# Performance work log

Hardware: AMD Instinct MI355X
Metric: run time of the kernel (lower is better)

## Reference

```python
import jax, jax.numpy as jnp
import numpy as np

B, D, H, E, NDIFF = 4096, 2048, 4096, 8, 3
TOPK = 2


def setup_inputs() -> dict:
    key = jax.random.key(0)
    ks = jax.random.split(key, 8)
    x = jax.random.normal(ks[0], (B, D), dtype=jnp.float32)
    difficulty_labels = jax.random.randint(ks[1], (B,), 0, NDIFF)
    emb = jax.random.normal(ks[2], (NDIFF, D), dtype=jnp.float32) * 0.02
    gate_W = jax.random.normal(ks[3], (E, 2 * D), dtype=jnp.float32) / np.sqrt(2.0 * D)
    gate_b = jnp.zeros((E,), dtype=jnp.float32)
    expert_W = jax.random.normal(ks[4], (E, H, D), dtype=jnp.float32) / np.sqrt(D)
    expert_b = jax.random.normal(ks[5], (E, H), dtype=jnp.float32) * 0.01
    return {"x": x, "difficulty_labels": difficulty_labels, "emb": emb,
            "gate_W": gate_W, "gate_b": gate_b,
            "expert_W": expert_W, "expert_b": expert_b}


def reference(x, difficulty_labels, emb, gate_W, gate_b, expert_W, expert_b):
    # gating: concat token features with difficulty embedding
    gate_in = jnp.concatenate([x, emb[difficulty_labels]], axis=1)       # [B, 2D]
    gate_logits = gate_in @ gate_W.T + gate_b                             # [B, E]
    topw, topk_idx = jax.lax.top_k(gate_logits, TOPK)                     # [B, 2]
    topk_probs = jax.nn.softmax(topw, axis=1)                             # [B, 2]
    # per-token combine weight for each expert (top-2 indices are distinct)
    combine = jnp.zeros((x.shape[0], E), dtype=x.dtype)
    combine = combine.at[jnp.arange(x.shape[0])[:, None], topk_idx].add(topk_probs)
    # dispatch/compute/combine: tokens with combine weight 0 contribute 0,
    # matching the masked gather/scatter-add of the original.
    out = jnp.zeros((x.shape[0], expert_W.shape[1]), dtype=x.dtype)
    for e in range(E):  # small fixed loop over experts
        y = x @ expert_W[e].T + expert_b[e]                               # [B, H]
        out = out + y * combine[:, e:e + 1]
    return (out, topk_idx)
```

## Files before the change

kernel.cpp:

```cpp
#include <hip/hip_runtime.h>
#include <hip/hip_bf16.h>

#define B_TOK 4096
#define DIM   2048
#define HID   4096
#define NEXP  8
#define CAP   4224

#define BM 128
#define BN 128
#define BK 64

typedef short  bf16x8 __attribute__((ext_vector_type(8)));
typedef unsigned short us16x8 __attribute__((ext_vector_type(8)));
typedef float  f32x4  __attribute__((ext_vector_type(4)));

__device__ __forceinline__ unsigned short f2bf(float f) {
    unsigned u = __builtin_bit_cast(unsigned, f);
    u += 0x7fffu + ((u >> 16) & 1u);
    return (unsigned short)(u >> 16);
}

__device__ __forceinline__ void async_copy16(const void* g, void* l) {
    __builtin_amdgcn_global_load_lds(
        (const __attribute__((address_space(1))) unsigned*)g,
        (__attribute__((address_space(3))) unsigned*)l, 16, 0, 0);
}

__global__ __launch_bounds__(256) void cvt_kernel(
    const float* __restrict__ src, unsigned short* __restrict__ dst, long n) {
    long i = ((long)blockIdx.x * 256 + threadIdx.x) * 8;
    if (i >= n) return;
    float4 v0 = *(const float4*)(src + i);
    float4 v1 = *(const float4*)(src + i + 4);
    us16x8 o = { f2bf(v0.x), f2bf(v0.y), f2bf(v0.z), f2bf(v0.w),
                 f2bf(v1.x), f2bf(v1.y), f2bf(v1.z), f2bf(v1.w) };
    *(us16x8*)(dst + i) = o;
}

__global__ __launch_bounds__(256) void compute_c_kernel(
    const float* __restrict__ emb, const float* __restrict__ gate_W,
    const float* __restrict__ gate_b, float* __restrict__ cbuf) {
    int wave = (blockIdx.x * blockDim.x + threadIdx.x) >> 6;
    int lane = threadIdx.x & 63;
    if (wave >= 24) return;
    int n = wave >> 3, e = wave & 7;
    const float4* er = (const float4*)(emb + (size_t)n * DIM);
    const float4* wr = (const float4*)(gate_W + (size_t)e * 2 * DIM + DIM);
    float acc = 0.f;
    for (int c = lane; c < DIM / 4; c += 64) {
        float4 a = er[c], b = wr[c];
        acc += a.x * b.x + a.y * b.y + a.z * b.z + a.w * b.w;
    }
    #pragma unroll
    for (int off = 32; off; off >>= 1) acc += __shfl_down(acc, off, 64);
    if (lane == 0) cbuf[n * 8 + e] = acc + gate_b[e];
}

__global__ __launch_bounds__(256) void gating_kernel(
    const float* __restrict__ x, const int* __restrict__ labels,
    const float* __restrict__ gate_W, const float* __restrict__ cbuf,
    int* __restrict__ counts, int* __restrict__ tlist,
    float* __restrict__ wlist, float* __restrict__ out_idx) {
    int wave = threadIdx.x >> 6, lane = threadIdx.x & 63;
    int b = blockIdx.x * 4 + wave;
    const float4* xr  = (const float4*)(x + (size_t)b * DIM);
    const float4* gw4 = (const float4*)gate_W;
    float acc[8] = {0.f, 0.f, 0.f, 0.f, 0.f, 0.f, 0.f, 0.f};
    for (int c = lane; c < DIM / 4; c += 64) {
        float4 xv = xr[c];
        #pragma unroll
        for (int e = 0; e < 8; ++e) {
            float4 wv = gw4[e * (2 * DIM / 4) + c];
            acc[e] += xv.x * wv.x + xv.y * wv.y + xv.z * wv.z + xv.w * wv.w;
        }
    }
    #pragma unroll
    for (int off = 32; off; off >>= 1) {
        #pragma unroll
        for (int e = 0; e < 8; ++e) acc[e] += __shfl_down(acc[e], off, 64);
    }
    if (lane == 0) {
        int lbl = labels[b];
        float lg[8];
        #pragma unroll
        for (int e = 0; e < 8; ++e) lg[e] = acc[e] + cbuf[lbl * 8 + e];
        int e0 = 0; float t0 = lg[0];
        #pragma unroll
        for (int e = 1; e < 8; ++e) if (lg[e] > t0) { t0 = lg[e]; e0 = e; }
        int e1 = -1; float t1 = -1e30f;
        #pragma unroll
        for (int e = 0; e < 8; ++e)
            if (e != e0 && lg[e] > t1) { t1 = lg[e]; e1 = e; }
        float w0 = 1.f / (1.f + __expf(t1 - t0));
        float w1 = 1.f - w0;
        int p0 = atomicAdd(&counts[e0], 1);
        int p1 = atomicAdd(&counts[e1], 1);
        tlist[e0 * CAP + p0] = b; wlist[e0 * CAP + p0] = w0;
        tlist[e1 * CAP + p1] = b; wlist[e1 * CAP + p1] = w1;
        out_idx[2 * b]     = (float)e0;
        out_idx[2 * b + 1] = (float)e1;
    }
}

__global__ void pad_kernel(const int* __restrict__ counts,
                           int* __restrict__ tlist, float* __restrict__ wlist) {
    int e = blockIdx.x, c = counts[e];
    int padded = (c + BM - 1) & ~(BM - 1);
    int i = c + threadIdx.x;
    if (i < padded) { tlist[e * CAP + i] = 0; wlist[e * CAP + i] = 0.f; }
}

__global__ __launch_bounds__(256) void moe_gemm_kernel(
    const unsigned short* __restrict__ xb, const unsigned short* __restrict__ Wb,
    const float* __restrict__ expert_b, const int* __restrict__ counts,
    const int* __restrict__ tlist, const float* __restrict__ wlist,
    float* __restrict__ out) {
    const int e  = blockIdx.z;
    const int m0 = blockIdx.y * BM;
    if (m0 >= counts[e]) return;
    const int n0 = blockIdx.x * BN;

    __shared__ unsigned short As[BM * BK];
    __shared__ unsigned short Bs[BN * BK];
    __shared__ int   toks[BM];
    __shared__ float wts[BM];

    const int t = threadIdx.x;
    if (t < BM) {
        toks[t] = tlist[e * CAP + m0 + t];
        wts[t]  = wlist[e * CAP + m0 + t];
    }
    __syncthreads();

    const int lane = t & 63, wave = t >> 6;
    const int rowc = lane >> 3;
    const int gsw  = ((lane & 7) ^ rowc) * 8;

    const unsigned short* gA[4];
    const unsigned short* gB[4];
    unsigned short* ldsA[4];
    unsigned short* ldsB[4];
    #pragma unroll
    for (int j = 0; j < 4; ++j) {
        int row = wave * 32 + j * 8 + rowc;
        gA[j] = xb + (size_t)toks[row] * DIM + gsw;
        gB[j] = Wb + ((size_t)e * HID + n0 + row) * DIM + gsw;
        ldsA[j] = As + (wave * 32 + j * 8) * BK;
        ldsB[j] = Bs + (wave * 32 + j * 8) * BK;
    }

    const int wm = wave >> 1, wn = wave & 1;
    const int r = lane & 15, quad = lane >> 4;

    f32x4 acc[4][4] = {};

    for (int k0 = 0; k0 < DIM; k0 += BK) {
        #pragma unroll
        for (int j = 0; j < 4; ++j) async_copy16(gA[j] + k0, ldsA[j]);
        #pragma unroll
        for (int j = 0; j < 4; ++j) async_copy16(gB[j] + k0, ldsB[j]);
        __syncthreads();
        #pragma unroll
        for (int kk = 0; kk < 2; ++kk) {
            bf16x8 af[4], bfr[4];
            const int pg = ((kk * 4 + quad) ^ (r & 7)) * 8;
            #pragma unroll
            for (int i = 0; i < 4; ++i) {
                af[i]  = *(const bf16x8*)&As[(wm * 64 + i * 16 + r) * BK + pg];
                bfr[i] = *(const bf16x8*)&Bs[(wn * 64 + i * 16 + r) * BK + pg];
            }
            #pragma unroll
            for (int im = 0; im < 4; ++im)
                #pragma unroll
                for (int in = 0; in < 4; ++in)
                    acc[im][in] = __builtin_amdgcn_mfma_f32_16x16x32_bf16(
                        af[im], bfr[in], acc[im][in], 0, 0, 0);
        }
        __syncthreads();
    }

    const float* eb = expert_b + (size_t)e * HID;
    #pragma unroll
    for (int in = 0; in < 4; ++in) {
        int col = n0 + wn * 64 + in * 16 + r;
        float bias = eb[col];
        #pragma unroll
        for (int im = 0; im < 4; ++im) {
            int rowb = wm * 64 + im * 16 + quad * 4;
            #pragma unroll
            for (int r4 = 0; r4 < 4; ++r4) {
                int row = rowb + r4;
                float w = wts[row];
                if (w != 0.f)
                    atomicAdd(out + (size_t)toks[row] * HID + col,
                              w * (acc[im][in][r4] + bias));
            }
        }
    }
}

extern "C" void kernel_launch(void* const* d_in, const int* in_sizes, int n_in,
                              void* d_out, int out_size, void* d_ws, size_t ws_size,
                              hipStream_t stream) {
    const float* x        = (const float*)d_in[0];
    const int*   labels   = (const int*)  d_in[1];
    const float* emb      = (const float*)d_in[2];
    const float* gate_W   = (const float*)d_in[3];
    const float* gate_b   = (const float*)d_in[4];
    const float* expert_W = (const float*)d_in[5];
    const float* expert_b = (const float*)d_in[6];
    float* out = (float*)d_out;

    char* ws = (char*)d_ws;
    int*   counts = (int*)ws;
    float* cbuf   = (float*)(ws + 128);
    int*   tlist  = (int*)(ws + 512);
    float* wlist  = (float*)(ws + 512 + NEXP * CAP * 4);
    unsigned short* xb = (unsigned short*)(ws + 512 + 2 * NEXP * CAP * 4);
    unsigned short* Wb = xb + (size_t)B_TOK * DIM;

    hipMemsetAsync(counts, 0, 8 * sizeof(int), stream);
    hipMemsetAsync(out, 0, (size_t)B_TOK * HID * sizeof(float), stream);

    cvt_kernel<<<(B_TOK * DIM) / (8 * 256), 256, 0, stream>>>(
        x, xb, (long)B_TOK * DIM);
    cvt_kernel<<<(NEXP * HID * DIM) / (8 * 256), 256, 0, stream>>>(
        expert_W, Wb, (long)NEXP * HID * DIM);
    compute_c_kernel<<<6, 256, 0, stream>>>(emb, gate_W, gate_b, cbuf);
    gating_kernel<<<B_TOK / 4, 256, 0, stream>>>(
        x, labels, gate_W, cbuf, counts, tlist, wlist,
        out + (size_t)B_TOK * HID);
    pad_kernel<<<NEXP, BM, 0, stream>>>(counts, tlist, wlist);
    moe_gemm_kernel<<<dim3(HID / BN, B_TOK / BM, NEXP), 256, 0, stream>>>(
        xb, Wb, expert_b, counts, tlist, wlist, out);
}
```

Measured before the change: 891.5 us.

## Replace atomic scatter-add with rank-slot stores plus combine kernel; double-buffer GEMM

The GEMM no longer atomically adds weighted results into a zeroed output. Each token's first-ranked expert result goes straight into out and its second into a y1 workspace, with padded rows sent to a trash buffer. A new combine kernel then applies bias and gating weights. The GEMM main loop also moves to BK=32 with double-buffered LDS staging and a launch-bounds occupancy hint. This removes the output memset and the fp32 atomics, at the cost of an extra 64MB buffer and a full read/write combine pass. The trash row is shared by all padded rows and written concurrently, which is a benign race.

```diff
diff --git a/kernel.cpp b/kernel.cpp
--- a/kernel.cpp
+++ b/kernel.cpp
@@ -9,7 +9,8 @@
 
 #define BM 128
 #define BN 128
-#define BK 64
+#define BK 32
+#define KITER (DIM / BK)
 
 typedef short  bf16x8 __attribute__((ext_vector_type(8)));
 typedef unsigned short us16x8 __attribute__((ext_vector_type(8)));
@@ -60,8 +61,10 @@
 __global__ __launch_bounds__(256) void gating_kernel(
     const float* __restrict__ x, const int* __restrict__ labels,
     const float* __restrict__ gate_W, const float* __restrict__ cbuf,
-    int* __restrict__ counts, int* __restrict__ tlist,
-    float* __restrict__ wlist, float* __restrict__ out_idx) {
+    int* __restrict__ counts, int* __restrict__ tlist, int* __restrict__ rlist,
+    float* __restrict__ wA, float* __restrict__ wB,
+    int* __restrict__ eA, int* __restrict__ eB,
+    float* __restrict__ out_idx) {
     int wave = threadIdx.x >> 6, lane = threadIdx.x & 63;
     int b = blockIdx.x * 4 + wave;
     const float4* xr  = (const float4*)(x + (size_t)b * DIM);
@@ -96,107 +99,141 @@
         float w1 = 1.f - w0;
         int p0 = atomicAdd(&counts[e0], 1);
         int p1 = atomicAdd(&counts[e1], 1);
-        tlist[e0 * CAP + p0] = b; wlist[e0 * CAP + p0] = w0;
-        tlist[e1 * CAP + p1] = b; wlist[e1 * CAP + p1] = w1;
+        tlist[e0 * CAP + p0] = b; rlist[e0 * CAP + p0] = 0;
+        tlist[e1 * CAP + p1] = b; rlist[e1 * CAP + p1] = 1;
+        wA[b] = w0; wB[b] = w1; eA[b] = e0; eB[b] = e1;
         out_idx[2 * b]     = (float)e0;
         out_idx[2 * b + 1] = (float)e1;
     }
 }
 
 __global__ void pad_kernel(const int* __restrict__ counts,
-                           int* __restrict__ tlist, float* __restrict__ wlist) {
+                           int* __restrict__ tlist, int* __restrict__ rlist) {
     int e = blockIdx.x, c = counts[e];
     int padded = (c + BM - 1) & ~(BM - 1);
     int i = c + threadIdx.x;
-    if (i < padded) { tlist[e * CAP + i] = 0; wlist[e * CAP + i] = 0.f; }
-}
-
-__global__ __launch_bounds__(256) void moe_gemm_kernel(
+    if (i < padded) { tlist[e * CAP + i] = 0; rlist[e * CAP + i] = 2; }
+}
+
+__global__ __launch_bounds__(256, 3) void moe_gemm_kernel(
     const unsigned short* __restrict__ xb, const unsigned short* __restrict__ Wb,
-    const float* __restrict__ expert_b, const int* __restrict__ counts,
-    const int* __restrict__ tlist, const float* __restrict__ wlist,
-    float* __restrict__ out) {
+    const int* __restrict__ counts, const int* __restrict__ tlist,
+    const int* __restrict__ rlist,
+    float* __restrict__ out0, float* __restrict__ y1, float* __restrict__ trash) {
     const int e  = blockIdx.z;
     const int m0 = blockIdx.y * BM;
     if (m0 >= counts[e]) return;
     const int n0 = blockIdx.x * BN;
 
-    __shared__ unsigned short As[BM * BK];
-    __shared__ unsigned short Bs[BN * BK];
-    __shared__ int   toks[BM];
-    __shared__ float wts[BM];
+    __shared__ unsigned short As0[BM * BK], As1[BM * BK];
+    __shared__ unsigned short Bs0[BN * BK], Bs1[BN * BK];
+    __shared__ int toks[BM];
+    __shared__ unsigned long long rowp[BM];
 
     const int t = threadIdx.x;
     if (t < BM) {
-        toks[t] = tlist[e * CAP + m0 + t];
-        wts[t]  = wlist[e * CAP + m0 + t];
+        int tok = tlist[e * CAP + m0 + t];
+        int rk  = rlist[e * CAP + m0 + t];
+        toks[t] = tok;
+        float* p = (rk == 0) ? out0 + (size_t)tok * HID
+                 : (rk == 1) ? y1   + (size_t)tok * HID
+                             : trash;
+        rowp[t] = (unsigned long long)p;
     }
     __syncthreads();
 
     const int lane = t & 63, wave = t >> 6;
-    const int rowc = lane >> 3;
-    const int gsw  = ((lane & 7) ^ rowc) * 8;
-
-    const unsigned short* gA[4];
-    const unsigned short* gB[4];
-    unsigned short* ldsA[4];
-    unsigned short* ldsB[4];
-    #pragma unroll
-    for (int j = 0; j < 4; ++j) {
-        int row = wave * 32 + j * 8 + rowc;
-        gA[j] = xb + (size_t)toks[row] * DIM + gsw;
-        gB[j] = Wb + ((size_t)e * HID + n0 + row) * DIM + gsw;
-        ldsA[j] = As + (wave * 32 + j * 8) * BK;
-        ldsB[j] = Bs + (wave * 32 + j * 8) * BK;
+    const int rowc = lane >> 2;
+    const int colg = lane & 3;
+    const int gcol = ((colg ^ (rowc & 3)) * 8);
+
+    const unsigned short* gA[2];
+    const unsigned short* gB[2];
+    int ldsoff[2];
+    #pragma unroll
+    for (int j = 0; j < 2; ++j) {
+        int row = wave * 32 + j * 16 + rowc;
+        gA[j] = xb + (size_t)toks[row] * DIM + gcol;
+        gB[j] = Wb + ((size_t)e * HID + n0 + row) * DIM + gcol;
+        ldsoff[j] = (wave * 32 + j * 16) * BK;
     }
 
     const int wm = wave >> 1, wn = wave & 1;
     const int r = lane & 15, quad = lane >> 4;
+    const int pg = (quad ^ (r & 3)) * 8;
 
     f32x4 acc[4][4] = {};
 
-    for (int k0 = 0; k0 < DIM; k0 += BK) {
-        #pragma unroll
-        for (int j = 0; j < 4; ++j) async_copy16(gA[j] + k0, ldsA[j]);
-        #pragma unroll
-        for (int j = 0; j < 4; ++j) async_copy16(gB[j] + k0, ldsB[j]);
+    auto stage = [&](unsigned short* Ad, unsigned short* Bd, int kstep) {
+        const int kc = kstep * BK;
+        #pragma unroll
+        for (int j = 0; j < 2; ++j) {
+            async_copy16(gA[j] + kc, Ad + ldsoff[j]);
+            async_copy16(gB[j] + kc, Bd + ldsoff[j]);
+        }
+    };
+    auto compute = [&](const unsigned short* Ab, const unsigned short* Bb) {
+        bf16x8 af[4], bfr[4];
+        #pragma unroll
+        for (int i = 0; i < 4; ++i) {
+            af[i]  = *(const bf16x8*)&Ab[(wm * 64 + i * 16 + r) * BK + pg];
+            bfr[i] = *(const bf16x8*)&Bb[(wn * 64 + i * 16 + r) * BK + pg];
+        }
+        #pragma unroll
+        for (int im = 0; im < 4; ++im)
+            #pragma unroll
+            for (int in = 0; in < 4; ++in)
+                acc[im][in] = __builtin_amdgcn_mfma_f32_16x16x32_bf16(
+                    af[im], bfr[in], acc[im][in], 0, 0, 0);
+    };
+
+    stage(As0, Bs0, 0);
+    __syncthreads();
+    for (int k2 = 0; k2 < KITER; k2 += 2) {
+        stage(As1, Bs1, k2 + 1);
+        compute(As0, Bs0);
         __syncthreads();
-        #pragma unroll
-        for (int kk = 0; kk < 2; ++kk) {
-            bf16x8 af[4], bfr[4];
-            const int pg = ((kk * 4 + quad) ^ (r & 7)) * 8;
-            #pragma unroll
-            for (int i = 0; i < 4; ++i) {
-                af[i]  = *(const bf16x8*)&As[(wm * 64 + i * 16 + r) * BK + pg];
-                bfr[i] = *(const bf16x8*)&Bs[(wn * 64 + i * 16 + r) * BK + pg];
-            }
-            #pragma unroll
-            for (int im = 0; im < 4; ++im)
-                #pragma unroll
-                for (int in = 0; in < 4; ++in)
-                    acc[im][in] = __builtin_amdgcn_mfma_f32_16x16x32_bf16(
-                        af[im], bfr[in], acc[im][in], 0, 0, 0);
-        }
+        if (k2 + 2 < KITER) stage(As0, Bs0, k2 + 2);
+        compute(As1, Bs1);
         __syncthreads();
     }
 
-    const float* eb = expert_b + (size_t)e * HID;
     #pragma unroll
     for (int in = 0; in < 4; ++in) {
         int col = n0 + wn * 64 + in * 16 + r;
-        float bias = eb[col];
         #pragma unroll
         for (int im = 0; im < 4; ++im) {
             int rowb = wm * 64 + im * 16 + quad * 4;
             #pragma unroll
             for (int r4 = 0; r4 < 4; ++r4) {
-                int row = rowb + r4;
-                float w = wts[row];
-                if (w != 0.f)
-                    atomicAdd(out + (size_t)toks[row] * HID + col,
-                              w * (acc[im][in][r4] + bias));
+                float* dst = (float*)rowp[rowb + r4];
+                dst[col] = acc[im][in][r4];
             }
         }
+    }
+}
+
+__global__ __launch_bounds__(256) void combine_kernel(
+    const float* __restrict__ y1, const float* __restrict__ eb,
+    const float* __restrict__ wA, const float* __restrict__ wB,
+    const int* __restrict__ eA, const int* __restrict__ eB,
+    float* __restrict__ out) {
+    int b = blockIdx.x;
+    float w0 = wA[b], w1 = wB[b];
+    int e0 = eA[b], e1 = eB[b];
+    const float4* y0r = (const float4*)(out + (size_t)b * HID);
+    const float4* y1r = (const float4*)(y1 + (size_t)b * HID);
+    const float4* b0r = (const float4*)(eb + (size_t)e0 * HID);
+    const float4* b1r = (const float4*)(eb + (size_t)e1 * HID);
+    float4* o = (float4*)(out + (size_t)b * HID);
+    for (int i = threadIdx.x; i < HID / 4; i += 256) {
+        float4 a = y0r[i], c = y1r[i], u = b0r[i], v = b1r[i];
+        float4 rs;
+        rs.x = w0 * (a.x + u.x) + w1 * (c.x + v.x);
+        rs.y = w0 * (a.y + u.y) + w1 * (c.y + v.y);
+        rs.z = w0 * (a.z + u.z) + w1 * (c.z + v.z);
+        rs.w = w0 * (a.w + u.w) + w1 * (c.w + v.w);
+        o[i] = rs;
     }
 }
 
@@ -214,14 +251,19 @@
 
     char* ws = (char*)d_ws;
     int*   counts = (int*)ws;
-    float* cbuf   = (float*)(ws + 128);
+    float* cbuf   = (float*)(ws + 256);
     int*   tlist  = (int*)(ws + 512);
-    float* wlist  = (float*)(ws + 512 + NEXP * CAP * 4);
-    unsigned short* xb = (unsigned short*)(ws + 512 + 2 * NEXP * CAP * 4);
+    int*   rlist  = (int*)(ws + 512 + 135168);
+    float* wA     = (float*)(ws + 270848);
+    float* wB     = (float*)(ws + 287232);
+    int*   eA     = (int*)  (ws + 303616);
+    int*   eB     = (int*)  (ws + 320000);
+    float* trash  = (float*)(ws + 336384);
+    float* y1     = (float*)(ws + 352768);
+    unsigned short* xb = (unsigned short*)(ws + 352768 + (size_t)B_TOK * HID * 4);
     unsigned short* Wb = xb + (size_t)B_TOK * DIM;
 
     hipMemsetAsync(counts, 0, 8 * sizeof(int), stream);
-    hipMemsetAsync(out, 0, (size_t)B_TOK * HID * sizeof(float), stream);
 
     cvt_kernel<<<(B_TOK * DIM) / (8 * 256), 256, 0, stream>>>(
         x, xb, (long)B_TOK * DIM);
@@ -229,9 +271,11 @@
         expert_W, Wb, (long)NEXP * HID * DIM);
     compute_c_kernel<<<6, 256, 0, stream>>>(emb, gate_W, gate_b, cbuf);
     gating_kernel<<<B_TOK / 4, 256, 0, stream>>>(
-        x, labels, gate_W, cbuf, counts, tlist, wlist,
+        x, labels, gate_W, cbuf, counts, tlist, rlist, wA, wB, eA, eB,
         out + (size_t)B_TOK * HID);
-    pad_kernel<<<NEXP, BM, 0, stream>>>(counts, tlist, wlist);
+    pad_kernel<<<NEXP, BM, 0, stream>>>(counts, tlist, rlist);
     moe_gemm_kernel<<<dim3(HID / BN, B_TOK / BM, NEXP), 256, 0, stream>>>(
-        xb, Wb, expert_b, counts, tlist, wlist, out);
-}
+        xb, Wb, counts, tlist, rlist, out, y1, trash);
+    combine_kernel<<<B_TOK, 256, 0, stream>>>(
+        y1, expert_b, wA, wB, eA, eB, out);
+}
```

New measurement: 751.3 us. -15.7%, faster.
